# Kernel optimization log

Hardware: AMD Instinct MI355X
Metric: run time of the kernel (lower is better)

The kernel has to match this reference:

```python
import jax, jax.numpy as jnp
import numpy as np

BATCH = 8192
GROUPS = 512
ARITY = 3
OUT_DIM = 8
ACT_FACTOR = 1.0


def setup_inputs() -> dict:
    key = jax.random.key(0)
    k1, k2 = jax.random.split(key)
    X = jax.random.normal(k1, (BATCH, GROUPS * ARITY), dtype=jnp.float32)
    params = jax.random.normal(k2, (GROUPS, 3 ** ARITY, OUT_DIM), dtype=jnp.float32)
    return {"X": X, "params": params}


def _high_order_act_b(A, params):
    # A: [B, G, r], params: [G, 3**r, D]
    r = A.shape[2]
    ref_ind = (3 ** r - 1) // 2  # sum_{i<r} 3**i
    A_abs = jnp.abs(A)
    A_ind = jnp.argsort(A_abs, axis=2)                      # [B,G,r] int
    A_sort = jnp.take_along_axis(A_abs, A_ind, axis=2)      # sorted |A|
    sgn = jnp.where(A >= 0, 1, -1).astype(jnp.int32)
    A_sgn = jnp.take_along_axis(sgn, A_ind, axis=2)         # signs in sorted order
    # simplex interpolation coefficients: smallest |A| then successive diffs
    coef = jnp.concatenate(
        [A_sort[:, :, :1], A_sort[:, :, 1:] - A_sort[:, :, :-1]], axis=2
    )  # [B,G,r]
    # base-3 index: suffix cumsum of sign * 3**orig_index, offset to center
    terms = A_sgn * (3 ** A_ind.astype(jnp.int32))
    params_A_ind = jnp.flip(jnp.cumsum(jnp.flip(terms, axis=2), axis=2), axis=2) + ref_ind  # [B,G,r]
    idx = jnp.transpose(params_A_ind, (1, 0, 2))            # [G,B,r]
    # gather params[g, idx[g,b,k], :] -> [G,B,r,D]
    gathered = jnp.take_along_axis(params[:, None, :, :], idx[..., None], axis=2)
    # einsum 'jikl,ijk->ijl' (torch) == 'gbrd,bgr->bgd'
    return jnp.einsum('gbrd,bgr->bgd', gathered, coef)


def reference(X, params):
    B = X.shape[0]
    A = X.reshape(B, GROUPS, ARITY)
    out1 = _high_order_act_b(A, params)                     # [B,G,D]
    return out1.reshape(B, GROUPS * OUT_DIM) * ACT_FACTOR
```

## Files before the change

kernel.cpp:

```cpp
#include <hip/hip_runtime.h>

typedef float vf4 __attribute__((ext_vector_type(4)));

#define BATCH  8192
#define GROUPS 512
#define OUT_D  8
#define GCH    32
#define NCH    (GROUPS / GCH)
#define RT     64
#define RW     16
#define PQ     54
#define LQ     55

__global__ __launch_bounds__(256) void hoact_kernel(
    const float* __restrict__ X,
    const float* __restrict__ P,
    float* __restrict__ out)
{
    __shared__ vf4 lp[GCH * LQ];

    const int chunk = blockIdx.x % NCH;
    const int rt    = blockIdx.x / NCH;

    const int tid  = threadIdx.x;
    const int lane = tid & 63;
    const int w    = tid >> 6;
    const int gsub = lane >> 1;
    const int h    = lane & 1;

    const vf4* P4 = (const vf4*)P + (size_t)chunk * (GCH * PQ);
    #pragma unroll
    for (int k = 0; k < 7; ++k) {
        int m = tid + 256 * k;
        if (m < GCH * PQ) {
            int gq = m / PQ;
            int iq = m - gq * PQ;
            lp[gq * LQ + iq] = P4[m];
        }
    }

    const int g = chunk * GCH + gsub;
    const int row0 = rt * RT + w * RW;
    const float* xcol = X + (size_t)g * 3 + (size_t)row0 * (GROUPS * 3);
    float xv[RW][3];
    #pragma unroll
    for (int it = 0; it < RW; ++it) {
        const float* xp = xcol + (size_t)it * (GROUPS * 3);
        xv[it][0] = xp[0];
        xv[it][1] = xp[1];
        xv[it][2] = xp[2];
    }

    __syncthreads();

    vf4* outb = (vf4*)out + (size_t)chunk * (GCH * OUT_D / 4) + lane
              + (size_t)row0 * (GROUPS * OUT_D / 4);
    const size_t row_u = GROUPS * OUT_D / 4;
    const int base = gsub * LQ + h;

    #pragma unroll
    for (int it = 0; it < RW; ++it) {
        float x0 = xv[it][0], x1 = xv[it][1], x2 = xv[it][2];

        float b0 = fabsf(x0), b1 = fabsf(x1), b2 = fabsf(x2);
        int t0 = (x0 >= 0.f) ? 1 : -1;
        int t1 = (x1 >= 0.f) ? 3 : -3;
        int t2 = (x2 >= 0.f) ? 9 : -9;
        if (b0 > b1) { float tb=b0; b0=b1; b1=tb; int tt=t0; t0=t1; t1=tt; }
        if (b1 > b2) { float tb=b1; b1=b2; b2=tb; int tt=t1; t1=t2; t2=tt; }
        if (b0 > b1) { float tb=b0; b0=b1; b1=tb; int tt=t0; t0=t1; t1=tt; }
        int i2 = t2 + 13;
        int i1 = t1 + t2 + 13;
        int i0 = t0 + t1 + t2 + 13;
        float c0 = b0;
        float c1 = b1 - b0;
        float c2 = b2 - b1;

        vf4 q0 = lp[base + i0 * 2];
        vf4 q1 = lp[base + i1 * 2];
        vf4 q2 = lp[base + i2 * 2];

        vf4 r = c0 * q0 + c1 * q1 + c2 * q2;

        outb[(size_t)it * row_u] = r;
    }
}

extern "C" void kernel_launch(void* const* d_in, const int* in_sizes, int n_in,
                              void* d_out, int out_size, void* d_ws, size_t ws_size,
                              hipStream_t stream) {
    const float* X = (const float*)d_in[0];
    const float* P = (const float*)d_in[1];
    float* out = (float*)d_out;

    const int grid = (BATCH / RT) * NCH;
    hoact_kernel<<<grid, 256, 0, stream>>>(X, P, out);
}
```

Measured before the change: 33.86 us.

## Widen group chunk to 64 with 512-thread blocks and nontemporal stores

```diff
diff --git a/kernel.cpp b/kernel.cpp
--- a/kernel.cpp
+++ b/kernel.cpp
@@ -5,14 +5,14 @@
 #define BATCH  8192
 #define GROUPS 512
 #define OUT_D  8
-#define GCH    32
+#define GCH    64
 #define NCH    (GROUPS / GCH)
 #define RT     64
-#define RW     16
+#define RW     8
 #define PQ     54
 #define LQ     55
 
-__global__ __launch_bounds__(256) void hoact_kernel(
+__global__ __launch_bounds__(512, 4) void hoact_kernel(
     const float* __restrict__ X,
     const float* __restrict__ P,
     float* __restrict__ out)
@@ -25,13 +25,11 @@
     const int tid  = threadIdx.x;
     const int lane = tid & 63;
     const int w    = tid >> 6;
-    const int gsub = lane >> 1;
-    const int h    = lane & 1;
 
     const vf4* P4 = (const vf4*)P + (size_t)chunk * (GCH * PQ);
     #pragma unroll
     for (int k = 0; k < 7; ++k) {
-        int m = tid + 256 * k;
+        int m = tid + 512 * k;
         if (m < GCH * PQ) {
             int gq = m / PQ;
             int iq = m - gq * PQ;
@@ -39,50 +37,62 @@
         }
     }
 
-    const int g = chunk * GCH + gsub;
+    const int gs0 = lane >> 1;
+    const int gs1 = gs0 + 32;
+    const int h   = lane & 1;
+
     const int row0 = rt * RT + w * RW;
-    const float* xcol = X + (size_t)g * 3 + (size_t)row0 * (GROUPS * 3);
-    float xv[RW][3];
+    const float* xb = X + (size_t)row0 * (GROUPS * 3) + (size_t)chunk * (GCH * 3);
+    float xv[RW][2][3];
     #pragma unroll
     for (int it = 0; it < RW; ++it) {
-        const float* xp = xcol + (size_t)it * (GROUPS * 3);
-        xv[it][0] = xp[0];
-        xv[it][1] = xp[1];
-        xv[it][2] = xp[2];
+        const float* xr = xb + (size_t)it * (GROUPS * 3);
+        const float* x0p = xr + gs0 * 3;
+        const float* x1p = xr + gs1 * 3;
+        xv[it][0][0] = x0p[0]; xv[it][0][1] = x0p[1]; xv[it][0][2] = x0p[2];
+        xv[it][1][0] = x1p[0]; xv[it][1][1] = x1p[1]; xv[it][1][2] = x1p[2];
     }
 
     __syncthreads();
 
-    vf4* outb = (vf4*)out + (size_t)chunk * (GCH * OUT_D / 4) + lane
-              + (size_t)row0 * (GROUPS * OUT_D / 4);
     const size_t row_u = GROUPS * OUT_D / 4;
-    const int base = gsub * LQ + h;
+    vf4* outb = (vf4*)out + (size_t)row0 * row_u
+              + (size_t)chunk * (GCH * OUT_D / 4) + lane;
+    const int base0 = gs0 * LQ + h;
+    const int base1 = gs1 * LQ + h;
 
     #pragma unroll
     for (int it = 0; it < RW; ++it) {
-        float x0 = xv[it][0], x1 = xv[it][1], x2 = xv[it][2];
+        vf4 res[2];
+        #pragma unroll
+        for (int sub = 0; sub < 2; ++sub) {
+            float x0 = xv[it][sub][0], x1 = xv[it][sub][1], x2 = xv[it][sub][2];
 
-        float b0 = fabsf(x0), b1 = fabsf(x1), b2 = fabsf(x2);
-        int t0 = (x0 >= 0.f) ? 1 : -1;
-        int t1 = (x1 >= 0.f) ? 3 : -3;
-        int t2 = (x2 >= 0.f) ? 9 : -9;
-        if (b0 > b1) { float tb=b0; b0=b1; b1=tb; int tt=t0; t0=t1; t1=tt; }
-        if (b1 > b2) { float tb=b1; b1=b2; b2=tb; int tt=t1; t1=t2; t2=tt; }
-        if (b0 > b1) { float tb=b0; b0=b1; b1=tb; int tt=t0; t0=t1; t1=tt; }
-        int i2 = t2 + 13;
-        int i1 = t1 + t2 + 13;
-        int i0 = t0 + t1 + t2 + 13;
-        float c0 = b0;
-        float c1 = b1 - b0;
-        float c2 = b2 - b1;
+            float b0 = fabsf(x0), b1 = fabsf(x1), b2 = fabsf(x2);
+            int t0 = (x0 >= 0.f) ? 1 : -1;
+            int t1 = (x1 >= 0.f) ? 3 : -3;
+            int t2 = (x2 >= 0.f) ? 9 : -9;
+            if (b0 > b1) { float tb=b0; b0=b1; b1=tb; int tt=t0; t0=t1; t1=tt; }
+            if (b1 > b2) { float tb=b1; b1=b2; b2=tb; int tt=t1; t1=t2; t2=tt; }
+            if (b0 > b1) { float tb=b0; b0=b1; b1=tb; int tt=t0; t0=t1; t1=tt; }
+            int i2 = t2 + 13;
+            int i1 = t1 + t2 + 13;
+            int i0 = t0 + t1 + t2 + 13;
+            float c0 = b0;
+            float c1 = b1 - b0;
+            float c2 = b2 - b1;
 
-        vf4 q0 = lp[base + i0 * 2];
-        vf4 q1 = lp[base + i1 * 2];
-        vf4 q2 = lp[base + i2 * 2];
+            const int base = sub ? base1 : base0;
+            vf4 q0 = lp[base + i0 * 2];
+            vf4 q1 = lp[base + i1 * 2];
+            vf4 q2 = lp[base + i2 * 2];
 
-        vf4 r = c0 * q0 + c1 * q1 + c2 * q2;
+            res[sub] = c0 * q0 + c1 * q1 + c2 * q2;
+        }
 
-        outb[(size_t)it * row_u] = r;
+        vf4* dst = outb + (size_t)it * row_u;
+        __builtin_nontemporal_store(res[0], dst);
+        __builtin_nontemporal_store(res[1], dst + 64);
     }
 }
 
@@ -94,5 +104,5 @@
     float* out = (float*)d_out;
 
     const int grid = (BATCH / RT) * NCH;
-    hoact_kernel<<<grid, 256, 0, stream>>>(X, P, out);
+    hoact_kernel<<<grid, 512, 0, stream>>>(X, P, out);
 }
```

Result: no change. 33.23 us (-1.9%).
